# Performance work log

Hardware: AMD Instinct MI355X
Metric: run time of the kernel (lower is better)

## Reference

```python
import jax, jax.numpy as jnp
import numpy as np

N = 4096
BATCH = 256
N_IO = 16
EPS = 1.1920929e-07  # torch RMSNorm default eps = finfo(float32).eps


def setup_inputs() -> dict:
    key = jax.random.key(0)
    k_x, k_w = jax.random.split(key)
    x_input = jax.random.normal(k_x, (BATCH, N), dtype=jnp.float32)
    # orthogonal init for W
    a = jax.random.normal(k_w, (N, N), dtype=jnp.float32)
    q, r = jnp.linalg.qr(a)
    W = q * jnp.sign(jnp.diag(r))[None, :]
    B = jnp.zeros((N,), dtype=jnp.float32)
    input_scale = jnp.ones((N_IO,), dtype=jnp.float32)
    output_scale = jnp.ones((N_IO,), dtype=jnp.float32)
    norm_weight = jnp.ones((N,), dtype=jnp.float32)  # RMSNorm elementwise affine
    input_pos = jnp.arange(N_IO, dtype=jnp.int32)            # ids 0..15
    output_pos = jnp.arange(N_IO, dtype=jnp.int32) + (N - N_IO)  # ids 4080..4095
    return {
        "x_input": x_input, "W": W, "B": B,
        "input_scale": input_scale, "output_scale": output_scale,
        "norm_weight": norm_weight,
        "input_pos": input_pos, "output_pos": output_pos,
        "steps": 16,
    }


def reference(x_input, W, B, input_scale, output_scale, norm_weight,
              input_pos, output_pos, steps):
    # dropout is identity in eval mode (rate 0.0)
    def step(h, inj):
        signal = h @ W + B + inj                      # [batch, N]
        a = jnp.tanh(signal)
        ms = jnp.mean(a * a, axis=-1, keepdims=True)
        return a * jax.lax.rsqrt(ms + EPS) * norm_weight

    # pulse mode: scaled input injected only at t == 0
    inj0 = x_input.at[:, input_pos].multiply(input_scale)
    h0 = jnp.zeros_like(x_input)                      # fresh state
    h1 = step(h0, inj0)

    def body(h, _):
        hn = step(h, 0.0)
        return hn, hn

    h_final, rest = jax.lax.scan(body, h1, None, length=steps - 1)  # rest: [steps-1, batch, N]
    outs = jnp.concatenate([h1[:, None, :], jnp.swapaxes(rest, 0, 1)], axis=1)  # [batch, steps, N]
    outs = outs.at[:, :, output_pos].multiply(output_scale)
    return outs, h_final
```

## Files before the change

kernel.cpp:

```cpp
#include <hip/hip_runtime.h>
#include <hip/hip_bf16.h>

#define BATCH 256
#define NDIM  4096
#define STEPS 16
#define EPS_RMS 1.1920929e-07f

typedef _Float16 f16x8 __attribute__((ext_vector_type(8)));
typedef float  f32x4  __attribute__((ext_vector_type(4)));
typedef unsigned short u16x4 __attribute__((ext_vector_type(4)));
typedef unsigned short u16x8 __attribute__((ext_vector_type(8)));

#define AS1 __attribute__((address_space(1)))
#define AS3 __attribute__((address_space(3)))
#define GLDS16(gp, lp) __builtin_amdgcn_global_load_lds( \
    (const AS1 void*)(gp), (AS3 void*)(lp), 16, 0, 0)
#define SBAR() do { asm volatile("" ::: "memory"); \
                    __builtin_amdgcn_s_barrier();  \
                    asm volatile("" ::: "memory"); } while (0)

__device__ __forceinline__ unsigned short f2h(float f) {
  _Float16 h = (_Float16)f;
  union { _Float16 h; unsigned short u; } v; v.h = h; return v.u;
}
__device__ __forceinline__ float h2f(unsigned short u) {
  union { unsigned short u; _Float16 h; } v; v.u = u; return (float)v.h;
}

__device__ __forceinline__ float block_reduce_sum_512(float v) {
  __shared__ float ws[8];
  __shared__ float tot;
  #pragma unroll
  for (int off = 32; off > 0; off >>= 1) v += __shfl_down(v, off, 64);
  int lane = threadIdx.x & 63, w = threadIdx.x >> 6;
  if (lane == 0) ws[w] = v;
  __syncthreads();
  if (threadIdx.x == 0) {
    float t = 0.f;
    #pragma unroll
    for (int i = 0; i < 8; ++i) t += ws[i];
    tot = t;
  }
  __syncthreads();
  return tot;
}

__global__ __launch_bounds__(256) void transpose_w(
    const float* __restrict__ W, unsigned short* __restrict__ Wt,
    const float* __restrict__ iscale, const float* __restrict__ oscale,
    const int* __restrict__ ipos, const int* __restrict__ opos,
    float* __restrict__ icm, float* __restrict__ ocm) {
  __shared__ float tile[64][65];
  int n0 = blockIdx.x * 64;
  int k0 = blockIdx.y * 64;
  int t = threadIdx.x;
  if (blockIdx.y == 0 && t < 64) {
    int c = n0 + t;
    float iv = 1.f, ov = 1.f;
    #pragma unroll
    for (int i = 0; i < 16; ++i) {
      if (ipos[i] == c) iv *= iscale[i];
      if (opos[i] == c) ov *= oscale[i];
    }
    icm[c] = iv; ocm[c] = ov;
  }
  int r = t >> 4, c4 = (t & 15) * 4;
  #pragma unroll
  for (int p = 0; p < 4; ++p) {
    f32x4 v = *(const f32x4*)(W + (size_t)(k0 + r + 16 * p) * NDIM + n0 + c4);
    tile[r + 16 * p][c4 + 0] = v[0];
    tile[r + 16 * p][c4 + 1] = v[1];
    tile[r + 16 * p][c4 + 2] = v[2];
    tile[r + 16 * p][c4 + 3] = v[3];
  }
  __syncthreads();
  #pragma unroll
  for (int p = 0; p < 4; ++p) {
    int nr = r + 16 * p;
    u16x4 o;
    #pragma unroll
    for (int j = 0; j < 4; ++j) o[j] = f2h(tile[c4 + j][nr]);
    *(u16x4*)(Wt + (size_t)(n0 + nr) * NDIM + k0 + c4) = o;
  }
}

__global__ __launch_bounds__(512) void step0_kernel(
    const float* __restrict__ x, const float* __restrict__ bias,
    const float* __restrict__ icm, const float* __restrict__ nw,
    unsigned short* __restrict__ hbuf) {
  int row = blockIdx.x;
  int tid = threadIdx.x;
  const float* xr = x + (size_t)row * NDIM;
  float a[8];
  float sq = 0.f;
  #pragma unroll
  for (int p = 0; p < 2; ++p) {
    int c = p * 2048 + tid * 4;
    f32x4 xv = *(const f32x4*)(xr + c);
    f32x4 bv = *(const f32x4*)(bias + c);
    f32x4 ic = *(const f32x4*)(icm + c);
    #pragma unroll
    for (int j = 0; j < 4; ++j) {
      float av = tanhf(bv[j] + xv[j] * ic[j]);
      a[p * 4 + j] = av;
      sq += av * av;
    }
  }
  float tot = block_reduce_sum_512(sq);
  float scale = rsqrtf(tot * (1.0f / NDIM) + EPS_RMS);
  unsigned short* hrow = hbuf + (size_t)row * NDIM;
  #pragma unroll
  for (int p = 0; p < 2; ++p) {
    int c = p * 2048 + tid * 4;
    f32x4 nv = *(const f32x4*)(nw + c);
    u16x4 hs;
    #pragma unroll
    for (int j = 0; j < 4; ++j) hs[j] = f2h(a[p * 4 + j] * scale * nv[j]);
    *(u16x4*)(hrow + c) = hs;
  }
}

__global__ __launch_bounds__(256, 2) void gemm_kernel(
    const unsigned short* __restrict__ A,
    const unsigned short* __restrict__ Bt,
    unsigned short* __restrict__ pbuf,
    const float* __restrict__ ocm,
    float* __restrict__ out, int tm1) {
  __shared__ __align__(16) unsigned short As[2][128 * 64];
  __shared__ __align__(16) unsigned short Bs[2][128 * 64];
  const int tid = threadIdx.x;
  const int n0 = blockIdx.x * 128;
  const int m0 = blockIdx.y * 128;
  const int ks = blockIdx.z;
  const int kbase = ks * 512;
  const int wave = tid >> 6, lane = tid & 63;
  const int wm = (wave >> 1) * 64, wn = (wave & 1) * 64;
  const int l15 = lane & 15;
  const int g = lane >> 4;
  const int q = l15 & 7;
  const int srow = tid >> 3;
  const int sch = tid & 7;
  const int koff = (sch ^ (srow & 7)) * 8;

  const unsigned short* aP[4];
  const unsigned short* bP[4];
  #pragma unroll
  for (int i = 0; i < 4; ++i) {
    aP[i] = A + (size_t)(m0 + i * 32 + srow) * NDIM + kbase + koff;
    bP[i] = Bt + (size_t)(n0 + i * 32 + srow) * NDIM + kbase + koff;
  }

  f32x4 acc[4][4];
  f32x4 zero = {0.f, 0.f, 0.f, 0.f};
  #pragma unroll
  for (int i = 0; i < 4; ++i)
    #pragma unroll
    for (int j = 0; j < 4; ++j) acc[i][j] = zero;

  #pragma unroll
  for (int i = 0; i < 4; ++i)
    GLDS16(aP[i], &As[0][(i * 32 + srow) * 64 + sch * 8]);
  #pragma unroll
  for (int i = 0; i < 4; ++i)
    GLDS16(bP[i], &Bs[0][(i * 32 + srow) * 64 + sch * 8]);

  for (int it = 0; it < 8; ++it) {
    const int p = it & 1;
    SBAR();
    if (it < 7) {
      const int kb = (it + 1) * 64;
      #pragma unroll
      for (int i = 0; i < 4; ++i)
        GLDS16(aP[i] + kb, &As[1 - p][(i * 32 + srow) * 64 + sch * 8]);
      #pragma unroll
      for (int i = 0; i < 4; ++i)
        GLDS16(bP[i] + kb, &Bs[1 - p][(i * 32 + srow) * 64 + sch * 8]);
      asm volatile("s_waitcnt vmcnt(8)" ::: "memory");
    } else {
      asm volatile("s_waitcnt vmcnt(0)" ::: "memory");
    }
    SBAR();
    #pragma unroll
    for (int kk = 0; kk < 2; ++kk) {
      f16x8 af[4], bfr[4];
      #pragma unroll
      for (int mf = 0; mf < 4; ++mf) {
        int row = wm + mf * 16 + l15;
        af[mf] = *(const f16x8*)&As[p][row * 64 + (((kk << 2) + g) ^ q) * 8];
      }
      #pragma unroll
      for (int nf = 0; nf < 4; ++nf) {
        int row = wn + nf * 16 + l15;
        bfr[nf] = *(const f16x8*)&Bs[p][row * 64 + (((kk << 2) + g) ^ q) * 8];
      }
      #pragma unroll
      for (int mf = 0; mf < 4; ++mf)
        #pragma unroll
        for (int nf = 0; nf < 4; ++nf)
          acc[mf][nf] = __builtin_amdgcn_mfma_f32_16x16x32_f16(af[mf], bfr[nf], acc[mf][nf], 0, 0, 0);
    }
  }

  {
    unsigned short* pout = pbuf + (size_t)ks * BATCH * NDIM;
    const int crow = g * 4;
    #pragma unroll
    for (int mf = 0; mf < 4; ++mf) {
      #pragma unroll
      for (int nf = 0; nf < 4; ++nf) {
        int col = n0 + wn + nf * 16 + l15;
        #pragma unroll
        for (int r = 0; r < 4; ++r) {
          int row = m0 + wm + mf * 16 + crow + r;
          pout[(size_t)row * NDIM + col] = f2h(acc[mf][nf][r]);
        }
      }
    }
  }

  {
    const int col0 = kbase + blockIdx.x * 16;
    const int row = m0 + (tid >> 1);
    const int c8 = (tid & 1) * 8;
    u16x8 hv = *(const u16x8*)(A + (size_t)row * NDIM + col0 + c8);
    f32x4 oc0 = *(const f32x4*)(ocm + col0 + c8);
    f32x4 oc1 = *(const f32x4*)(ocm + col0 + c8 + 4);
    f32x4 o0, o1;
    #pragma unroll
    for (int j = 0; j < 4; ++j) {
      o0[j] = h2f(hv[j]) * oc0[j];
      o1[j] = h2f(hv[j + 4]) * oc1[j];
    }
    float* orow = out + ((size_t)row * STEPS + tm1) * NDIM + col0 + c8;
    *(f32x4*)orow = o0;
    *(f32x4*)(orow + 4) = o1;
  }
}

__global__ __launch_bounds__(512) void normalize_kernel(
    const unsigned short* __restrict__ pbuf, const float* __restrict__ bias,
    const float* __restrict__ nw, const float* __restrict__ ocm,
    unsigned short* __restrict__ hbuf, float* __restrict__ out,
    float* __restrict__ hfin, int is_last) {
  const size_t SL = (size_t)BATCH * NDIM;
  int row = blockIdx.x;
  int tid = threadIdx.x;
  int c = tid * 8;
  const unsigned short* p0 = pbuf + (size_t)row * NDIM + c;
  float s[8];
  {
    const float* b0 = bias + c;
    #pragma unroll
    for (int j = 0; j < 8; ++j) s[j] = b0[j];
  }
  #pragma unroll
  for (int k = 0; k < 8; ++k) {
    u16x8 v = *(const u16x8*)(p0 + (size_t)k * SL);
    #pragma unroll
    for (int j = 0; j < 8; ++j) s[j] += h2f(v[j]);
  }
  float a[8];
  float sq = 0.f;
  #pragma unroll
  for (int j = 0; j < 8; ++j) {
    float av = tanhf(s[j]);
    a[j] = av;
    sq += av * av;
  }
  float tot = block_reduce_sum_512(sq);
  float scale = rsqrtf(tot * (1.0f / NDIM) + EPS_RMS);
  unsigned short* hrow = hbuf + (size_t)row * NDIM + c;
  const float* nv = nw + c;
  u16x8 hs;
  if (is_last) {
    float* orow = out + ((size_t)row * STEPS + (STEPS - 1)) * NDIM + c;
    float* frow = hfin + (size_t)row * NDIM + c;
    const float* oc = ocm + c;
    #pragma unroll
    for (int j = 0; j < 8; ++j) {
      float h = a[j] * scale * nv[j];
      hs[j] = f2h(h);
      orow[j] = h * oc[j];
      frow[j] = h;
    }
  } else {
    #pragma unroll
    for (int j = 0; j < 8; ++j) hs[j] = f2h(a[j] * scale * nv[j]);
  }
  *(u16x8*)hrow = hs;
}

extern "C" void kernel_launch(void* const* d_in, const int* in_sizes, int n_in,
                              void* d_out, int out_size, void* d_ws, size_t ws_size,
                              hipStream_t stream) {
  (void)in_sizes; (void)n_in; (void)out_size; (void)ws_size;
  const float* x      = (const float*)d_in[0];
  const float* W      = (const float*)d_in[1];
  const float* Bb     = (const float*)d_in[2];
  const float* iscale = (const float*)d_in[3];
  const float* oscale = (const float*)d_in[4];
  const float* nw     = (const float*)d_in[5];
  const int* ipos = (const int*)d_in[6];
  const int* opos = (const int*)d_in[7];

  char* ws = (char*)d_ws;
  unsigned short* Wt   = (unsigned short*)(ws);
  unsigned short* hA   = (unsigned short*)(ws + 33554432);
  unsigned short* hB   = (unsigned short*)(ws + 35651584);
  float* icm           = (float*)(ws + 37748736);
  float* ocm           = (float*)(ws + 37765120);
  unsigned short* pbuf = (unsigned short*)(ws + 37781504);

  float* out  = (float*)d_out;
  float* hfin = out + (size_t)BATCH * STEPS * NDIM;

  hipLaunchKernelGGL(transpose_w, dim3(64, 64), dim3(256), 0, stream,
                     W, Wt, iscale, oscale, ipos, opos, icm, ocm);
  hipLaunchKernelGGL(step0_kernel, dim3(256), dim3(512), 0, stream,
                     x, Bb, icm, nw, hA);
  for (int t = 1; t < STEPS; ++t) {
    const unsigned short* Ap = ((t - 1) & 1) ? hB : hA;
    unsigned short* Ac = (t & 1) ? hB : hA;
    hipLaunchKernelGGL(gemm_kernel, dim3(32, 2, 8), dim3(256), 0, stream,
                       Ap, Wt, pbuf, ocm, out, t - 1);
    hipLaunchKernelGGL(normalize_kernel, dim3(256), dim3(512), 0, stream,
                       pbuf, Bb, nw, ocm, Ac, out, hfin, (t == STEPS - 1) ? 1 : 0);
  }
}
```

Baseline: 339.1 us.

## Load A fragments directly from global into registers, bypassing LDS

The A operand tile is no longer staged through shared memory. Each wave now loads its own MFMA A fragments straight from global memory into registers, double-buffered across k-iterations, while B still goes through LDS. This cuts LDS traffic and footprint for A and removes the LDS reads for A fragments. In exchange, the two waves sharing the same rows each load A from global (duplicate loads), register pressure rises, and the vmcnt wait accounting changes.

```diff
diff --git a/kernel.cpp b/kernel.cpp
--- a/kernel.cpp
+++ b/kernel.cpp
@@ -126,7 +126,6 @@
     unsigned short* __restrict__ pbuf,
     const float* __restrict__ ocm,
     float* __restrict__ out, int tm1) {
-  __shared__ __align__(16) unsigned short As[2][128 * 64];
   __shared__ __align__(16) unsigned short Bs[2][128 * 64];
   const int tid = threadIdx.x;
   const int n0 = blockIdx.x * 128;
@@ -142,13 +141,15 @@
   const int sch = tid & 7;
   const int koff = (sch ^ (srow & 7)) * 8;
 
-  const unsigned short* aP[4];
   const unsigned short* bP[4];
   #pragma unroll
-  for (int i = 0; i < 4; ++i) {
-    aP[i] = A + (size_t)(m0 + i * 32 + srow) * NDIM + kbase + koff;
+  for (int i = 0; i < 4; ++i)
     bP[i] = Bt + (size_t)(n0 + i * 32 + srow) * NDIM + kbase + koff;
-  }
+
+  const unsigned short* aQ[4];
+  #pragma unroll
+  for (int mf = 0; mf < 4; ++mf)
+    aQ[mf] = A + (size_t)(m0 + wm + mf * 16 + l15) * NDIM + kbase + g * 8;
 
   f32x4 acc[4][4];
   f32x4 zero = {0.f, 0.f, 0.f, 0.f};
@@ -159,11 +160,15 @@
 
   #pragma unroll
   for (int i = 0; i < 4; ++i)
-    GLDS16(aP[i], &As[0][(i * 32 + srow) * 64 + sch * 8]);
-  #pragma unroll
-  for (int i = 0; i < 4; ++i)
     GLDS16(bP[i], &Bs[0][(i * 32 + srow) * 64 + sch * 8]);
-
+  f16x8 aCur[4][2], aNxt[4][2];
+  #pragma unroll
+  for (int mf = 0; mf < 4; ++mf)
+    #pragma unroll
+    for (int kk = 0; kk < 2; ++kk)
+      aCur[mf][kk] = *(const f16x8*)(aQ[mf] + kk * 32);
+
+  #pragma unroll
   for (int it = 0; it < 8; ++it) {
     const int p = it & 1;
     SBAR();
@@ -171,23 +176,20 @@
       const int kb = (it + 1) * 64;
       #pragma unroll
       for (int i = 0; i < 4; ++i)
-        GLDS16(aP[i] + kb, &As[1 - p][(i * 32 + srow) * 64 + sch * 8]);
-      #pragma unroll
-      for (int i = 0; i < 4; ++i)
         GLDS16(bP[i] + kb, &Bs[1 - p][(i * 32 + srow) * 64 + sch * 8]);
-      asm volatile("s_waitcnt vmcnt(8)" ::: "memory");
+      #pragma unroll
+      for (int mf = 0; mf < 4; ++mf)
+        #pragma unroll
+        for (int kk = 0; kk < 2; ++kk)
+          aNxt[mf][kk] = *(const f16x8*)(aQ[mf] + kb + kk * 32);
+      asm volatile("s_waitcnt vmcnt(12)" ::: "memory");
     } else {
       asm volatile("s_waitcnt vmcnt(0)" ::: "memory");
     }
     SBAR();
     #pragma unroll
     for (int kk = 0; kk < 2; ++kk) {
-      f16x8 af[4], bfr[4];
-      #pragma unroll
-      for (int mf = 0; mf < 4; ++mf) {
-        int row = wm + mf * 16 + l15;
-        af[mf] = *(const f16x8*)&As[p][row * 64 + (((kk << 2) + g) ^ q) * 8];
-      }
+      f16x8 bfr[4];
       #pragma unroll
       for (int nf = 0; nf < 4; ++nf) {
         int row = wn + nf * 16 + l15;
@@ -197,8 +199,13 @@
       for (int mf = 0; mf < 4; ++mf)
         #pragma unroll
         for (int nf = 0; nf < 4; ++nf)
-          acc[mf][nf] = __builtin_amdgcn_mfma_f32_16x16x32_f16(af[mf], bfr[nf], acc[mf][nf], 0, 0, 0);
-    }
+          acc[mf][nf] = __builtin_amdgcn_mfma_f32_16x16x32_f16(aCur[mf][kk], bfr[nf], acc[mf][nf], 0, 0, 0);
+    }
+    #pragma unroll
+    for (int mf = 0; mf < 4; ++mf)
+      #pragma unroll
+      for (int kk = 0; kk < 2; ++kk)
+        aCur[mf][kk] = aNxt[mf][kk];
   }
 
   {
```

New measurement: 464.0 us. 1.37x slower.
